# Kernel tuning notes

Measured on AMD Instinct MI355X. Metric: run time of the kernel, lower is better.

## Reference

```python
import jax, jax.numpy as jnp
import numpy as np

EPS = 1e-06


def setup_inputs() -> dict:
    key = jax.random.key(0)
    k1, k2 = jax.random.split(key)
    B, T, E = 4, 4096, 1024
    M = E // 2
    x = jax.random.normal(k1, (B, T, E), dtype=jnp.float32)
    # causal mask: position i may attend to j <= i... note module multiplies K
    # (which is nonzero only for j >= i) by mask; a standard causal lower-tri
    # mask would zero everything but the diagonal. The module's bump kernel
    # looks FORWARD (diff = (j-i).clamp(min=0)), so the natural mask here is
    # upper-triangular (j >= i), i.e. the 'causal' mask for this pooling.
    mask = jnp.triu(jnp.ones((T, T), dtype=bool))
    gate_raw = jnp.full((M,), -3.0, dtype=jnp.float32)
    return {"x": x, "mask": mask, "gate_raw": gate_raw}


def reference(x, mask, gate_raw):
    B, T, E = x.shape
    dtype = x.dtype
    x_c = x[..., 0::2]                                  # (B, T, M) content channels

    # convex bump kernel K[i, j], nonzero for j >= i
    i = jnp.arange(T, dtype=dtype)[:, None]
    j = jnp.arange(T, dtype=dtype)[None, :]
    diff = jnp.maximum(j - i, 0.0)
    horizon = jnp.maximum(jnp.float32(T) - i, 1.0)
    u = jnp.minimum(diff / horizon, 1.0 - EPS)
    K = jnp.exp(1.0 - 1.0 / (1.0 - u * u + EPS))
    K = jnp.where(u >= 1.0 - EPS, jnp.asarray(EPS, dtype), K)

    K = K * mask.astype(dtype)
    K = K / jnp.maximum(K.sum(-1, keepdims=True), EPS)  # row-normalize

    phi = jnp.einsum('ij,bjm->bim', K, x_c)             # (B, T, M)
    gate = jax.nn.softplus(gate_raw)[None, None, :]     # (1, 1, M)
    out = x.at[..., 1::2].set(phi * gate)               # write phase channels
    return out
```

## Files before the change

kernel.cpp:

```cpp
#include <hip/hip_runtime.h>
#include <cstdint>
#include <cstddef>

#define Tdim 4096
#define Bdim 4
#define Edim 1024
#define Mdim 512
#define EPSF 1e-6f
#define NTILES 1056

typedef __bf16 bf16x8 __attribute__((ext_vector_type(8)));
typedef float f32x4 __attribute__((ext_vector_type(4)));

__host__ __device__ __forceinline__ int panel_start(int p) { return p * (65 - p); }

__device__ __forceinline__ unsigned short f2bf(float f) {
  union { float f; unsigned int u; } a; a.f = f;
  unsigned int r = a.u + 0x7fffu + ((a.u >> 16) & 1u);
  return (unsigned short)(r >> 16);
}

__device__ __forceinline__ unsigned int pack_bf16(float a, float b) {
  union { float f; unsigned int u; } ua, ub; ua.f = a; ub.f = b;
  return __builtin_amdgcn_perm(ub.u + 0x8000u, ua.u + 0x8000u, 0x07060302u);
}

__device__ __forceinline__ float kernel_g(float dj, float inv_h) {
  float u = fminf(dj * inv_h, 1.0f - EPSF);
  return __expf(1.0f - 1.0f / (1.0f - u * u + EPSF));
}

typedef void __attribute__((address_space(1)))* gas1;
typedef void __attribute__((address_space(3)))* las3;
__device__ __forceinline__ void load_lds16(const void* g, void* l) {
  __builtin_amdgcn_global_load_lds((gas1)(g), (las3)(l), 16, 0, 0);
}

__global__ __launch_bounds__(256) void prep_kernel(const float* __restrict__ x,
                                                   float* __restrict__ inv_s,
                                                   unsigned short* __restrict__ XcT) {
  __shared__ float smem[1104];
  const int tid = threadIdx.x;
  const int id = blockIdx.x;
  if (id < Tdim) {
    const int i = id;
    const float inv_h = __fdividef(1.0f, (float)(Tdim - i));
    float s = 0.0f;
    for (int j = i + tid; j < Tdim; j += 256)
      s += kernel_g((float)(j - i), inv_h);
#pragma unroll
    for (int off = 32; off; off >>= 1) s += __shfl_down(s, off);
    if ((tid & 63) == 0) smem[1088 + (tid >> 6)] = s;
    __syncthreads();
    if (tid == 0)
      inv_s[i] = __fdividef(
          1.0f, fmaxf(smem[1088] + smem[1089] + smem[1090] + smem[1091], EPSF));
  } else {
    const int eid = id - Tdim;
    const int j0 = (eid & 63) * 64;
    const int m0 = ((eid >> 6) & 15) * 32;
    const int b  = eid >> 10;
    unsigned short* Ls = reinterpret_cast<unsigned short*>(smem);
    const int q = tid & 15;
    const int jbase = tid >> 4;
#pragma unroll
    for (int it = 0; it < 4; ++it) {
      const int jj = jbase + it * 16;
      const size_t off = ((size_t)(b * Tdim + j0 + jj)) * Edim + 2 * m0 + 4 * q;
      const float4 v = *reinterpret_cast<const float4*>(&x[off]);
      Ls[(2 * q) * 68 + jj]     = f2bf(v.x);
      Ls[(2 * q + 1) * 68 + jj] = f2bf(v.z);
    }
    __syncthreads();
    const int ch = tid & 15;
    const int mb = tid >> 4;
#pragma unroll
    for (int it = 0; it < 2; ++it) {
      const int m = mb + it * 16;
      ushort4 uv;
      uv.x = Ls[m * 68 + 4 * ch];
      uv.y = Ls[m * 68 + 4 * ch + 1];
      uv.z = Ls[m * 68 + 4 * ch + 2];
      uv.w = Ls[m * 68 + 4 * ch + 3];
      *reinterpret_cast<ushort4*>(
          &XcT[((size_t)(b * Mdim + m0 + m)) * Tdim + j0 + 4 * ch]) = uv;
    }
  }
}

__global__ __launch_bounds__(256) void packK_kernel(const float* __restrict__ inv_s,
                                                    unsigned short* __restrict__ Kswz) {
  const int id = blockIdx.x;
  int p = 0;
  while (id >= (p + 1) * (64 - p)) ++p;
  const int jt = id - panel_start(p);
  const int i0 = p * 128;
  const int jb0 = i0 + jt * 64;
  unsigned short* dst = Kswz + (size_t)id * 8192;
  const int tid = threadIdx.x;
#pragma unroll
  for (int ss = 0; ss < 4; ++ss) {
    const int G = ss * 256 + tid;
    const int lane = G & 63;
    const int kk = (G >> 6) & 1;
    const int r  = (G >> 7) & 3;
    const int h  = G >> 9;
    const int li = h * 64 + r * 16 + (lane & 15);
    const int i  = i0 + li;
    const float inv_h = __fdividef(1.0f, (float)(Tdim - i));
    const float sinv = inv_s[i];
    const int jb = jb0 + (kk * 4 + (lane >> 4)) * 8;
    float v[8];
#pragma unroll
    for (int e = 0; e < 8; ++e) {
      const int j = jb + e;
      v[e] = (j >= i) ? kernel_g((float)(j - i), inv_h) * sinv : 0.0f;
    }
    uint4 pk;
    pk.x = pack_bf16(v[0], v[1]);
    pk.y = pack_bf16(v[2], v[3]);
    pk.z = pack_bf16(v[4], v[5]);
    pk.w = pack_bf16(v[6], v[7]);
    *reinterpret_cast<uint4*>(&dst[(size_t)G * 8]) = pk;
  }
}

__global__ __launch_bounds__(256) void gemm_kernel(
    const unsigned short* __restrict__ Kswz,
    const unsigned short* __restrict__ XcT,
    const float* __restrict__ x,
    const float* __restrict__ graw,
    float* __restrict__ out) {
  __shared__ unsigned short Bs[2][128 * 64];
  const int id = blockIdx.x;
  int p;
  if (id < 256) p = id >> 4;
  else          p = 31 - ((id - 256) >> 4);
  const int mb = id & 15;
  const int i0 = p * 128;
  const int m0 = (mb & 3) * 128;
  const int b  = mb >> 2;
  const int tid = threadIdx.x;
  const int w = tid >> 6;
  const int l = tid & 63;
  const int wr = w >> 1, wc = w & 1;
  const unsigned short* Brow = XcT + ((size_t)b * Mdim + m0) * Tdim;
  const int srow  = l >> 3;
  const int sslot = l & 7;
  const int schunk = (sslot ^ srow) * 8;
  const unsigned short* Apan =
      Kswz + (size_t)panel_start(p) * 8192 + (size_t)(wr * 8) * 512 + (size_t)l * 8;

  f32x4 acc[4][4] = {};
  const int n = (Tdim - i0) >> 6;

#pragma unroll
  for (int t = 0; t < 4; ++t) {
    const int rr = (w * 4 + t) * 8 + srow;
    load_lds16(Brow + (size_t)rr * Tdim + (i0 + schunk), &Bs[0][(w * 4 + t) * 512]);
  }

  const int lr16 = l & 15;
  const int kq = l >> 4;
  int cur = 0;
  for (int t = 0; t < n; ++t, cur ^= 1) {
    __syncthreads();
    const unsigned short* At = Apan + (size_t)t * 8192;
    bf16x8 af[2][4];
#pragma unroll
    for (int r = 0; r < 4; ++r) {
      af[0][r] = *reinterpret_cast<const bf16x8*>(At + (r * 2 + 0) * 512);
      af[1][r] = *reinterpret_cast<const bf16x8*>(At + (r * 2 + 1) * 512);
    }
    __builtin_amdgcn_sched_barrier(0);
    if (t + 1 < n) {
      const int jn = i0 + (t + 1) * 64;
#pragma unroll
      for (int q = 0; q < 4; ++q) {
        const int rr = (w * 4 + q) * 8 + srow;
        load_lds16(Brow + (size_t)rr * Tdim + (jn + schunk), &Bs[cur ^ 1][(w * 4 + q) * 512]);
      }
    }
#pragma unroll
    for (int kk = 0; kk < 2; ++kk) {
      bf16x8 bfr[4];
      const int chunk = kk * 4 + kq;
      const int slot = (chunk ^ (lr16 & 7)) * 8;
#pragma unroll
      for (int c = 0; c < 4; ++c)
        bfr[c] = *reinterpret_cast<const bf16x8*>(&Bs[cur][(wc * 64 + c * 16 + lr16) * 64 + slot]);
#pragma unroll
      for (int r = 0; r < 4; ++r)
#pragma unroll
        for (int c = 0; c < 4; ++c)
          acc[r][c] = __builtin_amdgcn_mfma_f32_16x16x32_bf16(af[kk][r], bfr[c], acc[r][c], 0, 0, 0);
    }
  }

  const int lr = l & 15;
  const int lq = l >> 4;
  float gm[4];
#pragma unroll
  for (int c = 0; c < 4; ++c) {
    const float v = graw[m0 + wc * 64 + c * 16 + lr];
    gm[c] = fmaxf(v, 0.0f) + __logf(1.0f + __expf(-fabsf(v)));
  }
#pragma unroll
  for (int r = 0; r < 4; ++r) {
    const int ii = i0 + wr * 64 + r * 16 + lq * 4;
#pragma unroll
    for (int c = 0; c < 4; ++c) {
      const int m = m0 + wc * 64 + c * 16 + lr;
#pragma unroll
      for (int v = 0; v < 4; ++v) {
        const size_t o = ((size_t)(b * Tdim + ii + v)) * Edim + 2 * m;
        const float2 xv = *reinterpret_cast<const float2*>(&x[o]);
        float2 res;
        res.x = xv.x;
        res.y = acc[r][c][v] * gm[c];
        *reinterpret_cast<float2*>(&out[o]) = res;
      }
    }
  }
}

__global__ __launch_bounds__(256) void fallback_kernel(const float* __restrict__ x,
                                                       const float* __restrict__ graw,
                                                       float* __restrict__ out) {
  const int i = blockIdx.x, b = blockIdx.y, tid = threadIdx.x;
  const float inv_h = 1.0f / (float)(Tdim - i);
  float s = 0.0f;
  for (int j = i + tid; j < Tdim; j += 256)
    s += kernel_g((float)(j - i), inv_h);
#pragma unroll
  for (int off = 32; off; off >>= 1) s += __shfl_down(s, off);
  __shared__ float red[4];
  __shared__ float sinv_sh;
  if ((tid & 63) == 0) red[tid >> 6] = s;
  __syncthreads();
  if (tid == 0) sinv_sh = 1.0f / (red[0] + red[1] + red[2] + red[3]);
  __syncthreads();
  const float sinv = sinv_sh;
  const float* xb = x + (size_t)b * Tdim * Edim;
  float a0 = 0.0f, a1 = 0.0f;
  const int m0 = tid, m1 = tid + 256;
  for (int j = i; j < Tdim; ++j) {
    const float wgt = kernel_g((float)(j - i), inv_h);
    const float* xr = xb + (size_t)j * Edim;
    a0 += wgt * xr[2 * m0];
    a1 += wgt * xr[2 * m1];
  }
  const float v0 = graw[m0], v1 = graw[m1];
  const float g0 = fmaxf(v0, 0.0f) + log1pf(__expf(-fabsf(v0)));
  const float g1 = fmaxf(v1, 0.0f) + log1pf(__expf(-fabsf(v1)));
  const size_t o = ((size_t)(b * Tdim + i)) * Edim;
  const float* xi = xb + (size_t)i * Edim;
  out[o + 2 * m0]     = xi[2 * m0];
  out[o + 2 * m0 + 1] = a0 * sinv * g0;
  out[o + 2 * m1]     = xi[2 * m1];
  out[o + 2 * m1 + 1] = a1 * sinv * g1;
}

extern "C" void kernel_launch(void* const* d_in, const int* in_sizes, int n_in,
                              void* d_out, int out_size, void* d_ws, size_t ws_size,
                              hipStream_t stream) {
  const float* x = (const float*)d_in[0];
  const float* gate_raw = (const float*)d_in[2];
  float* out = (float*)d_out;

  const size_t XcT_bytes  = (size_t)Bdim * Mdim * Tdim * 2;
  const size_t Kswz_bytes = (size_t)NTILES * 16384;
  const size_t inv_bytes  = (size_t)Tdim * 4;
  const size_t need = XcT_bytes + Kswz_bytes + inv_bytes;

  if (ws_size < need) {
    fallback_kernel<<<dim3(Tdim, Bdim), 256, 0, stream>>>(x, gate_raw, out);
    return;
  }

  char* ws = (char*)d_ws;
  unsigned short* XcT  = (unsigned short*)ws;
  unsigned short* Kswz = (unsigned short*)(ws + XcT_bytes);
  float* inv_s         = (float*)(ws + XcT_bytes + Kswz_bytes);

  prep_kernel<<<dim3(2 * Tdim), 256, 0, stream>>>(x, inv_s, XcT);
  packK_kernel<<<dim3(NTILES), 256, 0, stream>>>(inv_s, Kswz);
  gemm_kernel<<<dim3(512), 256, 0, stream>>>(Kswz, XcT, x, gate_raw, out);
}
```

Measured before the change: 227.5 us.

## Triple-buffer B tiles in LDS and register-prefetch A fragments one step ahead

The GEMM main loop moves from double-buffered to triple-buffered LDS for the X tiles, issuing loads two steps ahead. A fragments are now prefetched into alternating register sets one iteration early, and an explicit vmcnt wait replaces the full __syncthreads. The goal is to hide global-load latency behind MFMA work. In exchange it uses more LDS and registers, relies on a hand-tuned vmcnt count, and issues clamped redundant loads at the tail. The loop is unrolled by two, which assumes n is even; n is a multiple of 2 since (4096-i0)/64 with i0 a multiple of 128.

New measurement: 221.6 us. 1.03x faster.

```diff
diff --git a/kernel.cpp b/kernel.cpp
--- a/kernel.cpp
+++ b/kernel.cpp
@@ -131,7 +131,7 @@
     const float* __restrict__ x,
     const float* __restrict__ graw,
     float* __restrict__ out) {
-  __shared__ unsigned short Bs[2][128 * 64];
+  __shared__ unsigned short Bs[3][128 * 64];
   const int id = blockIdx.x;
   int p;
   if (id < 256) p = id >> 4;
@@ -153,49 +153,80 @@
 
   f32x4 acc[4][4] = {};
   const int n = (Tdim - i0) >> 6;
-
-#pragma unroll
-  for (int t = 0; t < 4; ++t) {
-    const int rr = (w * 4 + t) * 8 + srow;
-    load_lds16(Brow + (size_t)rr * Tdim + (i0 + schunk), &Bs[0][(w * 4 + t) * 512]);
-  }
-
   const int lr16 = l & 15;
   const int kq = l >> 4;
-  int cur = 0;
-  for (int t = 0; t < n; ++t, cur ^= 1) {
-    __syncthreads();
-    const unsigned short* At = Apan + (size_t)t * 8192;
-    bf16x8 af[2][4];
-#pragma unroll
-    for (int r = 0; r < 4; ++r) {
-      af[0][r] = *reinterpret_cast<const bf16x8*>(At + (r * 2 + 0) * 512);
-      af[1][r] = *reinterpret_cast<const bf16x8*>(At + (r * 2 + 1) * 512);
-    }
-    __builtin_amdgcn_sched_barrier(0);
-    if (t + 1 < n) {
-      const int jn = i0 + (t + 1) * 64;
-#pragma unroll
-      for (int q = 0; q < 4; ++q) {
-        const int rr = (w * 4 + q) * 8 + srow;
-        load_lds16(Brow + (size_t)rr * Tdim + (jn + schunk), &Bs[cur ^ 1][(w * 4 + q) * 512]);
-      }
-    }
-#pragma unroll
-    for (int kk = 0; kk < 2; ++kk) {
-      bf16x8 bfr[4];
-      const int chunk = kk * 4 + kq;
-      const int slot = (chunk ^ (lr16 & 7)) * 8;
-#pragma unroll
-      for (int c = 0; c < 4; ++c)
-        bfr[c] = *reinterpret_cast<const bf16x8*>(&Bs[cur][(wc * 64 + c * 16 + lr16) * 64 + slot]);
-#pragma unroll
-      for (int r = 0; r < 4; ++r)
-#pragma unroll
-        for (int c = 0; c < 4; ++c)
-          acc[r][c] = __builtin_amdgcn_mfma_f32_16x16x32_bf16(af[kk][r], bfr[c], acc[r][c], 0, 0, 0);
-    }
-  }
+
+#pragma unroll
+  for (int q = 0; q < 4; ++q) {
+    const int rr = (w * 4 + q) * 8 + srow;
+    load_lds16(Brow + (size_t)rr * Tdim + (i0 + schunk), &Bs[0][(w * 4 + q) * 512]);
+  }
+  asm volatile("" ::: "memory");
+  bf16x8 af0[2][4], af1[2][4];
+#pragma unroll
+  for (int r = 0; r < 4; ++r) {
+    af0[0][r] = *reinterpret_cast<const bf16x8*>(Apan + (r * 2 + 0) * 512);
+    af0[1][r] = *reinterpret_cast<const bf16x8*>(Apan + (r * 2 + 1) * 512);
+  }
+  asm volatile("" ::: "memory");
+#pragma unroll
+  for (int q = 0; q < 4; ++q) {
+    const int rr = (w * 4 + q) * 8 + srow;
+    load_lds16(Brow + (size_t)rr * Tdim + (i0 + 64 + schunk), &Bs[1][(w * 4 + q) * 512]);
+  }
+
+#define GHALF(tc, afC, afN)                                                       \
+  do {                                                                            \
+    asm volatile("s_waitcnt vmcnt(12)" ::: "memory");                             \
+    __builtin_amdgcn_s_barrier();                                                 \
+    __builtin_amdgcn_sched_barrier(0);                                            \
+                       \
+    const int tpre = ((tc) + 1 < n) ? (tc) + 1 : n - 1;                           \
+    const unsigned short* Ap = Apan + (size_t)tpre * 8192;                        \
+    _Pragma("unroll")                                                             \
+    for (int r = 0; r < 4; ++r) {                                                 \
+      afN[0][r] = *reinterpret_cast<const bf16x8*>(Ap + (r * 2 + 0) * 512);       \
+      afN[1][r] = *reinterpret_cast<const bf16x8*>(Ap + (r * 2 + 1) * 512);       \
+    }                                                                             \
+              \
+    {                                                                             \
+      const int ts = (tc) + 2;                                                    \
+      const int jn = i0 + (((ts) < n) ? (ts) : n - 1) * 64;                       \
+      unsigned short* bdst = Bs[(ts) % 3];                                        \
+      _Pragma("unroll")                                                           \
+      for (int q = 0; q < 4; ++q) {                                               \
+        const int rr = (w * 4 + q) * 8 + srow;                                    \
+        load_lds16(Brow + (size_t)rr * Tdim + (jn + schunk),                      \
+                   &bdst[(w * 4 + q) * 512]);                                     \
+      }                                                                           \
+    }                                                                             \
+                                         \
+    {                                                                             \
+      const unsigned short* bsrc = Bs[(tc) % 3];                                  \
+      _Pragma("unroll")                                                           \
+      for (int kk = 0; kk < 2; ++kk) {                                            \
+        bf16x8 bfr[4];                                                            \
+        const int chunk = kk * 4 + kq;                                            \
+        const int slot = (chunk ^ (lr16 & 7)) * 8;                \
+        _Pragma("unroll")                                                         \
+        for (int c = 0; c < 4; ++c)                                               \
+          bfr[c] = *reinterpret_cast<const bf16x8*>(                              \
+              &bsrc[(wc * 64 + c * 16 + lr16) * 64 + slot]);                      \
+        _Pragma("unroll")                                                         \
+        for (int r = 0; r < 4; ++r)                                               \
+          _Pragma("unroll")                                                       \
+          for (int c = 0; c < 4; ++c)                                             \
+            acc[r][c] = __builtin_amdgcn_mfma_f32_16x16x32_bf16(                  \
+                afC[kk][r], bfr[c], acc[r][c], 0, 0, 0);                          \
+      }                                                                           \
+    }                                                                             \
+  } while (0)
+
+  for (int t = 0; t < n; t += 2) {
+    GHALF(t, af0, af1);
+    GHALF(t + 1, af1, af0);
+  }
+#undef GHALF
 
   const int lr = l & 15;
   const int lq = l >> 4;
```

## Load B fragments directly from global into registers, dropping LDS staging

Applied to the files above, without the earlier changes.

The GEMM no longer stages the X^T tile in LDS with async global-to-LDS loads and per-step barriers. Each lane now reads its B fragments straight from global memory into registers, using a two-deep software pipeline over half-k-steps (ping-pong register buffers). This removes the __syncthreads and LDS traffic, but the B tile is now fetched redundantly by the two waves that share a column block. It also relies on L2/cache to absorb the uncoalesced 16-byte row reads.

After: 248.0 us. 1.09x slower.

```diff
diff --git a/kernel.cpp b/kernel.cpp
--- a/kernel.cpp
+++ b/kernel.cpp
@@ -28,12 +28,6 @@
 __device__ __forceinline__ float kernel_g(float dj, float inv_h) {
   float u = fminf(dj * inv_h, 1.0f - EPSF);
   return __expf(1.0f - 1.0f / (1.0f - u * u + EPSF));
-}
-
-typedef void __attribute__((address_space(1)))* gas1;
-typedef void __attribute__((address_space(3)))* las3;
-__device__ __forceinline__ void load_lds16(const void* g, void* l) {
-  __builtin_amdgcn_global_load_lds((gas1)(g), (las3)(l), 16, 0, 0);
 }
 
 __global__ __launch_bounds__(256) void prep_kernel(const float* __restrict__ x,
@@ -131,7 +125,6 @@
     const float* __restrict__ x,
     const float* __restrict__ graw,
     float* __restrict__ out) {
-  __shared__ unsigned short Bs[2][128 * 64];
   const int id = blockIdx.x;
   int p;
   if (id < 256) p = id >> 4;
@@ -144,58 +137,53 @@
   const int w = tid >> 6;
   const int l = tid & 63;
   const int wr = w >> 1, wc = w & 1;
-  const unsigned short* Brow = XcT + ((size_t)b * Mdim + m0) * Tdim;
-  const int srow  = l >> 3;
-  const int sslot = l & 7;
-  const int schunk = (sslot ^ srow) * 8;
+  const int lr16 = l & 15;
+  const int kq = l >> 4;
+
   const unsigned short* Apan =
       Kswz + (size_t)panel_start(p) * 8192 + (size_t)(wr * 8) * 512 + (size_t)l * 8;
+  const unsigned short* Bbase =
+      XcT + ((size_t)b * Mdim + m0 + wc * 64 + lr16) * Tdim;
 
   f32x4 acc[4][4] = {};
   const int n = (Tdim - i0) >> 6;
-
-#pragma unroll
-  for (int t = 0; t < 4; ++t) {
-    const int rr = (w * 4 + t) * 8 + srow;
-    load_lds16(Brow + (size_t)rr * Tdim + (i0 + schunk), &Bs[0][(w * 4 + t) * 512]);
-  }
-
-  const int lr16 = l & 15;
-  const int kq = l >> 4;
-  int cur = 0;
-  for (int t = 0; t < n; ++t, cur ^= 1) {
-    __syncthreads();
-    const unsigned short* At = Apan + (size_t)t * 8192;
-    bf16x8 af[2][4];
-#pragma unroll
-    for (int r = 0; r < 4; ++r) {
-      af[0][r] = *reinterpret_cast<const bf16x8*>(At + (r * 2 + 0) * 512);
-      af[1][r] = *reinterpret_cast<const bf16x8*>(At + (r * 2 + 1) * 512);
-    }
-    __builtin_amdgcn_sched_barrier(0);
-    if (t + 1 < n) {
-      const int jn = i0 + (t + 1) * 64;
-#pragma unroll
-      for (int q = 0; q < 4; ++q) {
-        const int rr = (w * 4 + q) * 8 + srow;
-        load_lds16(Brow + (size_t)rr * Tdim + (jn + schunk), &Bs[cur ^ 1][(w * 4 + q) * 512]);
-      }
-    }
-#pragma unroll
-    for (int kk = 0; kk < 2; ++kk) {
-      bf16x8 bfr[4];
-      const int chunk = kk * 4 + kq;
-      const int slot = (chunk ^ (lr16 & 7)) * 8;
-#pragma unroll
-      for (int c = 0; c < 4; ++c)
-        bfr[c] = *reinterpret_cast<const bf16x8*>(&Bs[cur][(wc * 64 + c * 16 + lr16) * 64 + slot]);
-#pragma unroll
-      for (int r = 0; r < 4; ++r)
-#pragma unroll
-        for (int c = 0; c < 4; ++c)
-          acc[r][c] = __builtin_amdgcn_mfma_f32_16x16x32_bf16(af[kk][r], bfr[c], acc[r][c], 0, 0, 0);
-    }
-  }
+  const int nk = n << 1;
+
+#define LOADSTEP(s_, af_, bf_)                                                   \
+  do {                                                                           \
+    const int t_ = (s_) >> 1, kk_ = (s_) & 1;                                    \
+    const unsigned short* Ap_ = Apan + (size_t)t_ * 8192 + (size_t)kk_ * 512;    \
+    _Pragma("unroll")                                                            \
+    for (int r = 0; r < 4; ++r)                                                  \
+      af_[r] = *reinterpret_cast<const bf16x8*>(Ap_ + r * 1024);                 \
+    const size_t joff_ = (size_t)(i0 + (s_) * 32 + kq * 8);                      \
+    _Pragma("unroll")                                                            \
+    for (int c = 0; c < 4; ++c)                                                  \
+      bf_[c] = *reinterpret_cast<const bf16x8*>(Bbase + (size_t)c * (16 * Tdim)  \
+                                                + joff_);                        \
+  } while (0)
+
+#define MFMASTEP(af_, bf_)                                                       \
+  do {                                                                           \
+    _Pragma("unroll")                                                            \
+    for (int r = 0; r < 4; ++r)                                                  \
+      _Pragma("unroll")                                                          \
+      for (int c = 0; c < 4; ++c)                                                \
+        acc[r][c] = __builtin_amdgcn_mfma_f32_16x16x32_bf16(af_[r], bf_[c],      \
+                                                            acc[r][c], 0, 0, 0); \
+  } while (0)
+
+  bf16x8 afA[4], bfA[4], afB[4], bfB[4];
+  LOADSTEP(0, afA, bfA);
+  for (int s = 0; s < nk; s += 2) {
+    LOADSTEP(s + 1, afB, bfB);
+    MFMASTEP(afA, bfA);
+    const int s2 = (s + 2 < nk) ? s + 2 : nk - 1;
+    LOADSTEP(s2, afA, bfA);
+    MFMASTEP(afB, bfB);
+  }
+#undef LOADSTEP
+#undef MFMASTEP
 
   const int lr = l & 15;
   const int lq = l >> 4;
```
